# Optimization experiments

Measured on AMD Instinct MI355X. Metric: run time of the kernel, lower is better.

## Reference

```python
import jax, jax.numpy as jnp
import numpy as np

N_USER = 100000
N_ITEM = 50000
EMB = 64
LAYERS = 3
N_INTER = 2000000
BATCH = 4096


def setup_inputs() -> dict:
    key = jax.random.key(0)
    ks = jax.random.split(key, 12)
    N = N_USER + N_ITEM
    # bipartite interactions u -> i, symmetrized
    u = jax.random.randint(ks[0], (N_INTER,), 0, N_USER, dtype=jnp.int32)
    i = jax.random.randint(ks[1], (N_INTER,), 0, N_ITEM, dtype=jnp.int32) + N_USER
    edge_src = jnp.concatenate([u, i])
    edge_dst = jnp.concatenate([i, u])
    # symmetric normalization D^-1/2 A D^-1/2 (as in getSparseGraph)
    deg = jnp.bincount(edge_dst, length=N).astype(jnp.float32)
    d_inv_sqrt = jnp.where(deg > 0, jax.lax.rsqrt(jnp.maximum(deg, 1.0)), 0.0)
    edge_w = d_inv_sqrt[edge_src] * d_inv_sqrt[edge_dst]
    s = 1.0 / np.sqrt(EMB)  # xavier-ish scale
    inp = {
        "user_emb": jax.random.normal(ks[2], (N_USER, EMB), jnp.float32) * s,
        "item_emb": jax.random.normal(ks[3], (N_ITEM, EMB), jnp.float32) * s,
        "W_gc": jax.random.normal(ks[4], (LAYERS, EMB, EMB), jnp.float32) * s,
        "b_gc": jax.random.normal(ks[5], (LAYERS, 1, EMB), jnp.float32) * s,
        "W_bi": jax.random.normal(ks[6], (LAYERS, EMB, EMB), jnp.float32) * s,
        "b_bi": jax.random.normal(ks[7], (LAYERS, 1, EMB), jnp.float32) * s,
        "edge_w": edge_w,
        "edge_src": edge_src,
        "edge_dst": edge_dst,
        "users": jax.random.randint(ks[8], (BATCH,), 0, N_USER, dtype=jnp.int64),
        "pos_items": jax.random.randint(ks[9], (BATCH,), 0, N_ITEM, dtype=jnp.int64),
        "neg_items": jax.random.randint(ks[10], (BATCH,), 0, N_ITEM, dtype=jnp.int64),
    }
    return inp


def reference(user_emb, item_emb, W_gc, b_gc, W_bi, b_bi, edge_w,
              edge_src, edge_dst, users, pos_items, neg_items):
    n_user = user_emb.shape[0]
    N = n_user + item_emb.shape[0]
    ego = jnp.concatenate([user_emb, item_emb], axis=0)  # [N, d]
    all_embeddings = [ego]
    for k in range(W_gc.shape[0]):
        # SpMM: side = A_hat @ ego  (gather + weighted scatter-add)
        side = jax.ops.segment_sum(ego[edge_src] * edge_w[:, None], edge_dst,
                                   num_segments=N)
        sum_e = side @ W_gc[k] + b_gc[k]
        bi_e = (ego * side) @ W_bi[k] + b_bi[k]
        ego = jax.nn.leaky_relu(sum_e + bi_e, negative_slope=0.2)
        # dropout omitted (eval mode / identity for deterministic baseline)
        nrm = jnp.linalg.norm(ego, axis=1, keepdims=True)
        all_embeddings.append(ego / jnp.maximum(nrm, 1e-12))
    all_e = jnp.concatenate(all_embeddings, axis=1)  # [N, (L+1)*d]
    u_g = all_e[:n_user][users]
    i_g = all_e[n_user:]
    return (u_g, i_g[pos_items], i_g[neg_items])
```

## Files before the change

kernel.cpp:

```cpp
#include <hip/hip_runtime.h>

#define EMB 64
#define B2SHIFT 8
#define B2ROWS 256
#define MAXB 1024

typedef short v8s __attribute__((ext_vector_type(8)));
typedef float v4f __attribute__((ext_vector_type(4)));

__device__ __forceinline__ float b2f(unsigned short u) {
    return __uint_as_float(((unsigned int)u) << 16);
}
__device__ __forceinline__ unsigned short f2b(float f) {
    unsigned int u = __float_as_uint(f);
    u += 0x7FFF + ((u >> 16) & 1);
    return (unsigned short)(u >> 16);
}

__global__ void k_init_ego(const float* __restrict__ user_emb,
                           const float* __restrict__ item_emb,
                           const float* __restrict__ dsq,
                           unsigned short* __restrict__ egob,
                           unsigned short* __restrict__ egow,
                           unsigned short* __restrict__ all_eb,
                           int n_user, int N) {
    int idx = blockIdx.x * blockDim.x + threadIdx.x;
    int total = N * EMB;
    if (idx >= total) return;
    int n = idx >> 6;
    int c = idx & 63;
    float v = (n < n_user) ? user_emb[idx] : item_emb[(size_t)(n - n_user) * EMB + c];
    unsigned short b = f2b(v);
    egob[idx] = b;
    egow[idx] = f2b(dsq[n] * v);
    __builtin_nontemporal_store(b, &all_eb[(size_t)n * 256 + c]);
}

__global__ __launch_bounds__(256) void k_bhist(const int* __restrict__ dst,
                                               int* __restrict__ bins,
                                               int M, int nb2) {
    __shared__ int h[MAXB];
    for (int i = threadIdx.x; i < nb2; i += 256) h[i] = 0;
    __syncthreads();
    for (int e = blockIdx.x * 256 + threadIdx.x; e < M; e += gridDim.x * 256)
        atomicAdd(&h[dst[e] >> B2SHIFT], 1);
    __syncthreads();
    for (int i = threadIdx.x; i < nb2; i += 256)
        if (h[i]) atomicAdd(&bins[i], h[i]);
}

__global__ __launch_bounds__(1024) void k_bscan(const int* __restrict__ bins,
                                                int* __restrict__ boff,
                                                int* __restrict__ bcur,
                                                int* __restrict__ row_ptr,
                                                int P, int N) {
    __shared__ int buf[1024];
    int tid = threadIdx.x;
    int v = (tid < P) ? bins[tid] : 0;
    buf[tid] = v;
    __syncthreads();
    for (int d = 1; d < 1024; d <<= 1) {
        int add = (tid >= d) ? buf[tid - d] : 0;
        __syncthreads();
        buf[tid] += add;
        __syncthreads();
    }
    if (tid < P) {
        int excl = buf[tid] - v;
        boff[tid] = excl;
        bcur[tid] = excl;
    }
    if (tid == P - 1) {
        boff[P] = buf[tid];
        row_ptr[N] = buf[tid];
    }
}

__global__ __launch_bounds__(256) void k_bin(const int* __restrict__ src,
                                             const int* __restrict__ dst,
                                             int* __restrict__ bcur,
                                             int* __restrict__ binned,
                                             int M, int nb2) {
    __shared__ int hist[MAXB];
    __shared__ int runcur[MAXB];
    int chunk = (M + gridDim.x - 1) / gridDim.x;
    int lo = blockIdx.x * chunk;
    int hi = min(lo + chunk, M);
    for (int i = threadIdx.x; i < nb2; i += 256) hist[i] = 0;
    __syncthreads();
    for (int e = lo + threadIdx.x; e < hi; e += 256)
        atomicAdd(&hist[dst[e] >> B2SHIFT], 1);
    __syncthreads();
    for (int i = threadIdx.x; i < nb2; i += 256) {
        int c = hist[i];
        runcur[i] = c ? atomicAdd(&bcur[i], c) : 0;
    }
    __syncthreads();
    for (int e = lo + threadIdx.x; e < hi; e += 256) {
        int d = dst[e];
        int pos = atomicAdd(&runcur[d >> B2SHIFT], 1);
        binned[pos] = (src[e] << B2SHIFT) | (d & (B2ROWS - 1));
    }
}

__global__ __launch_bounds__(256) void k_csrb(const int* __restrict__ boff,
                                              const int* __restrict__ binned,
                                              int* __restrict__ row_ptr,
                                              float* __restrict__ dsq,
                                              int* __restrict__ csr, int N) {
    __shared__ int hist[B2ROWS];
    __shared__ int scan[B2ROWS];
    int b = blockIdx.x;
    int beg = boff[b], end = boff[b + 1];
    int tid = threadIdx.x;
    hist[tid] = 0;
    __syncthreads();
    for (int e = beg + tid; e < end; e += 256)
        atomicAdd(&hist[binned[e] & (B2ROWS - 1)], 1);
    __syncthreads();
    int c = hist[tid];
    scan[tid] = c;
    __syncthreads();
    for (int d = 1; d < B2ROWS; d <<= 1) {
        int add = (tid >= d) ? scan[tid - d] : 0;
        __syncthreads();
        scan[tid] += add;
        __syncthreads();
    }
    int excl = beg + scan[tid] - c;
    int node = (b << B2SHIFT) + tid;
    if (node < N) {
        row_ptr[node] = excl;
        dsq[node] = (c > 0) ? rsqrtf((float)c) : 0.0f;
    }
    __syncthreads();
    hist[tid] = excl;
    __syncthreads();
    for (int e = beg + tid; e < end; e += 256) {
        int v = binned[e];
        int pos = atomicAdd(&hist[v & (B2ROWS - 1)], 1);
        csr[pos] = v >> B2SHIFT;
    }
}

__global__ __launch_bounds__(256) void k_side(const int* __restrict__ row_ptr,
                                              const int* __restrict__ csr,
                                              const float* __restrict__ dsq,
                                              const unsigned short* __restrict__ egow,
                                              const unsigned short* __restrict__ egob,
                                              unsigned short* __restrict__ X, int N) {
    int wave = threadIdx.x >> 6;
    int lane = threadIdx.x & 63;
    int n = blockIdx.x * 4 + wave;
    if (n >= N) return;
    int beg = __builtin_amdgcn_readfirstlane(row_ptr[n]);
    int end = __builtin_amdgcn_readfirstlane(row_ptr[n + 1]);
    float a0 = 0.f, a1 = 0.f, a2 = 0.f, a3 = 0.f;
    int e = beg;
    while (e < end) {
        int take = end - e;
        if (take > 64) take = 64;
        int vidx = csr[min(e + lane, end - 1)];
        int j = 0;
        for (; j + 16 <= take; j += 16) {
            int s[16];
#pragma unroll
            for (int u = 0; u < 16; u++)
                s[u] = __builtin_amdgcn_readlane(vidx, j + u);
            float v[16];
#pragma unroll
            for (int u = 0; u < 16; u++)
                v[u] = b2f(egow[(size_t)s[u] * EMB + lane]);
#pragma unroll
            for (int u = 0; u < 16; u += 4) {
                a0 += v[u + 0];
                a1 += v[u + 1];
                a2 += v[u + 2];
                a3 += v[u + 3];
            }
        }
        for (; j + 8 <= take; j += 8) {
            int s0 = __builtin_amdgcn_readlane(vidx, j + 0);
            int s1 = __builtin_amdgcn_readlane(vidx, j + 1);
            int s2 = __builtin_amdgcn_readlane(vidx, j + 2);
            int s3 = __builtin_amdgcn_readlane(vidx, j + 3);
            int s4 = __builtin_amdgcn_readlane(vidx, j + 4);
            int s5 = __builtin_amdgcn_readlane(vidx, j + 5);
            int s6 = __builtin_amdgcn_readlane(vidx, j + 6);
            int s7 = __builtin_amdgcn_readlane(vidx, j + 7);
            float v0 = b2f(egow[(size_t)s0 * EMB + lane]);
            float v1 = b2f(egow[(size_t)s1 * EMB + lane]);
            float v2 = b2f(egow[(size_t)s2 * EMB + lane]);
            float v3 = b2f(egow[(size_t)s3 * EMB + lane]);
            float v4 = b2f(egow[(size_t)s4 * EMB + lane]);
            float v5 = b2f(egow[(size_t)s5 * EMB + lane]);
            float v6 = b2f(egow[(size_t)s6 * EMB + lane]);
            float v7 = b2f(egow[(size_t)s7 * EMB + lane]);
            a0 += v0 + v4;
            a1 += v1 + v5;
            a2 += v2 + v6;
            a3 += v3 + v7;
        }
        for (; j < take; j++) {
            int s = __builtin_amdgcn_readlane(vidx, j);
            a0 += b2f(egow[(size_t)s * EMB + lane]);
        }
        e += take;
    }
    float s = dsq[n] * ((a0 + a1) + (a2 + a3));
    float eg = b2f(egob[(size_t)n * EMB + lane]);
    X[(size_t)n * 128 + lane] = f2b(s);
    X[(size_t)n * 128 + 64 + lane] = f2b(s * eg);
}

__global__ __launch_bounds__(256, 2) void k_mt(
        const unsigned short* __restrict__ X,
        unsigned short* __restrict__ egob, unsigned short* __restrict__ egow,
        const float* __restrict__ dsq,
        const float* __restrict__ Wgc, const float* __restrict__ bgc,
        const float* __restrict__ Wbi, const float* __restrict__ bbi,
        unsigned short* __restrict__ all_eb, int N, int layer_col) {
    __shared__ unsigned short sWT[64 * 136];
    __shared__ float sB[64];
    int tid = threadIdx.x;
    for (int i = tid; i < 64 * 64; i += 256) {
        int k = i >> 6, n = i & 63;
        sWT[n * 136 + k]      = f2b(Wgc[i]);
        sWT[n * 136 + 64 + k] = f2b(Wbi[i]);
    }
    if (tid < 64) sB[tid] = bgc[tid] + bbi[tid];
    __syncthreads();

    int wave = tid >> 6, lane = tid & 63;
    int q = lane >> 4, col = lane & 15;

    v8s Bf[4][4];
#pragma unroll
    for (int nt = 0; nt < 4; nt++)
#pragma unroll
        for (int kt = 0; kt < 4; kt++)
            Bf[nt][kt] = *(const v8s*)&sWT[(nt * 16 + col) * 136 + kt * 32 + q * 8];

    int nrt = (N + 15) >> 4;
    int rt0 = (blockIdx.x * 4 + wave) * 4;
    int rt1 = min(rt0 + 4, nrt);
    for (int t = rt0; t < rt1; t++) {
        int r0 = t << 4;
        int rowA = min(r0 + col, N - 1);
        v8s Af[4];
#pragma unroll
        for (int kt = 0; kt < 4; kt++)
            Af[kt] = *(const v8s*)&X[(size_t)rowA * 128 + kt * 32 + q * 8];
        v4f acc[4];
#pragma unroll
        for (int nt = 0; nt < 4; nt++) {
            float b = sB[nt * 16 + col];
            acc[nt] = (v4f){b, b, b, b};
        }
#pragma unroll
        for (int kt = 0; kt < 4; kt++)
#pragma unroll
            for (int nt = 0; nt < 4; nt++)
                acc[nt] = __builtin_amdgcn_mfma_f32_16x16x32_bf16(
                    Af[kt], Bf[nt][kt], acc[nt], 0, 0, 0);
#pragma unroll
        for (int reg = 0; reg < 4; reg++) {
            int row = r0 + q * 4 + reg;
            float v[4];
            float ssq = 0.f;
#pragma unroll
            for (int nt = 0; nt < 4; nt++) {
                float x = acc[nt][reg];
                x = x > 0.f ? x : 0.2f * x;
                v[nt] = x;
                ssq += x * x;
            }
            ssq += __shfl_xor(ssq, 1, 64);
            ssq += __shfl_xor(ssq, 2, 64);
            ssq += __shfl_xor(ssq, 4, 64);
            ssq += __shfl_xor(ssq, 8, 64);
            float inv = 1.0f / fmaxf(sqrtf(ssq), 1e-12f);
            if (row < N) {
                float dn = dsq[row];
#pragma unroll
                for (int nt = 0; nt < 4; nt++) {
                    int c = nt * 16 + col;
                    egob[(size_t)row * EMB + c] = f2b(v[nt]);
                    egow[(size_t)row * EMB + c] = f2b(v[nt] * dn);
                    __builtin_nontemporal_store(
                        f2b(v[nt] * inv),
                        &all_eb[(size_t)row * 256 + layer_col + c]);
                }
            }
        }
    }
}

__global__ void k_gather(const unsigned short* __restrict__ all_eb,
                         const int* __restrict__ users,
                         const int* __restrict__ pos,
                         const int* __restrict__ neg,
                         float* __restrict__ out, int n_user, int batch) {
    int idx = blockIdx.x * blockDim.x + threadIdx.x;
    int total = batch * 256;
    if (idx >= 3 * total) return;
    int which = idx / total;
    int r = idx - which * total;
    int b = r >> 8;
    int c = r & 255;
    int node;
    if (which == 0) node = users[b];
    else if (which == 1) node = n_user + pos[b];
    else node = n_user + neg[b];
    out[idx] = b2f(all_eb[(size_t)node * 256 + c]);
}

static inline size_t align256(size_t x) { return (x + 255) & ~(size_t)255; }

extern "C" void kernel_launch(void* const* d_in, const int* in_sizes, int n_in,
                              void* d_out, int out_size, void* d_ws, size_t ws_size,
                              hipStream_t stream) {
    const float* user_emb = (const float*)d_in[0];
    const float* item_emb = (const float*)d_in[1];
    const float* W_gc = (const float*)d_in[2];
    const float* b_gc = (const float*)d_in[3];
    const float* W_bi = (const float*)d_in[4];
    const float* b_bi = (const float*)d_in[5];
    const int* edge_src = (const int*)d_in[7];
    const int* edge_dst = (const int*)d_in[8];
    const int* users = (const int*)d_in[9];
    const int* pos = (const int*)d_in[10];
    const int* neg = (const int*)d_in[11];

    int n_user = in_sizes[0] / EMB;
    int n_item = in_sizes[1] / EMB;
    int N = n_user + n_item;
    int M = in_sizes[6];
    int layers = in_sizes[2] / (EMB * EMB);
    int batch = in_sizes[9];
    float* out = (float*)d_out;

    int nb2 = (N + B2ROWS - 1) >> B2SHIFT;
    int nrt = (N + 15) >> 4;

    char* p = (char*)d_ws;
    unsigned short* egob = (unsigned short*)p;   p += align256((size_t)N * EMB * 2);
    unsigned short* egow = (unsigned short*)p;   p += align256((size_t)N * EMB * 2);
    unsigned short* X = (unsigned short*)p;      p += align256((size_t)N * 128 * 2);
    unsigned short* all_eb = (unsigned short*)p; p += align256((size_t)N * 256 * 2);
    float* dsq = (float*)p;            p += align256((size_t)N * 4);
    int* row_ptr = (int*)p;            p += align256((size_t)(N + 1) * 4);
    int* bins = (int*)p;               p += align256((size_t)nb2 * 4);
    int* boff = (int*)p;               p += align256((size_t)(nb2 + 1) * 4);
    int* bcur = (int*)p;               p += align256((size_t)nb2 * 4);
    int* binned = (int*)p;             p += align256((size_t)M * 4);
    int* csr = (int*)p;                p += align256((size_t)M * 4);

    hipMemsetAsync(bins, 0, (size_t)nb2 * 4, stream);

    k_bhist<<<512, 256, 0, stream>>>(edge_dst, bins, M, nb2);
    k_bscan<<<1, 1024, 0, stream>>>(bins, boff, bcur, row_ptr, nb2, N);
    k_bin<<<512, 256, 0, stream>>>(edge_src, edge_dst, bcur, binned, M, nb2);
    k_csrb<<<nb2, 256, 0, stream>>>(boff, binned, row_ptr, dsq, csr, N);

    k_init_ego<<<(N * EMB + 255) / 256, 256, 0, stream>>>(
        user_emb, item_emb, dsq, egob, egow, all_eb, n_user, N);

    for (int k = 0; k < layers; k++) {
        k_side<<<(N + 3) / 4, 256, 0, stream>>>(row_ptr, csr, dsq, egow, egob, X, N);
        k_mt<<<(nrt + 15) / 16, 256, 0, stream>>>(
            X, egob, egow, dsq,
            W_gc + (size_t)k * EMB * EMB, b_gc + (size_t)k * EMB,
            W_bi + (size_t)k * EMB * EMB, b_bi + (size_t)k * EMB,
            all_eb, N, (k + 1) * EMB);
    }

    k_gather<<<(3 * batch * 256 + 255) / 256, 256, 0, stream>>>(
        all_eb, users, pos, neg, out, n_user, batch);
}
```

Measured before the change: 605.7 us.

## Gather four neighbor rows per wave with 8-byte loads in SpMM

The SpMM gather kernel now splits each wave into four 16-lane groups. Each group loads a different neighbor row as uint2 (four bf16 values per lane) instead of each lane loading one 2-byte element of a single row. Partial sums are combined with cross-group shuffles, and 16 lanes write packed outputs. The aim is fewer, wider memory instructions and more gathers in flight, at the cost of shuffles, masking for partial groups, and a final reduction.

```diff
diff --git a/kernel.cpp b/kernel.cpp
--- a/kernel.cpp
+++ b/kernel.cpp
@@ -10,6 +10,12 @@
 
 __device__ __forceinline__ float b2f(unsigned short u) {
     return __uint_as_float(((unsigned int)u) << 16);
+}
+__device__ __forceinline__ float b2f_lo(unsigned int u) {
+    return __uint_as_float(u << 16);
+}
+__device__ __forceinline__ float b2f_hi(unsigned int u) {
+    return __uint_as_float(u & 0xFFFF0000u);
 }
 __device__ __forceinline__ unsigned short f2b(float f) {
     unsigned int u = __float_as_uint(f);
@@ -155,62 +161,64 @@
     if (n >= N) return;
     int beg = __builtin_amdgcn_readfirstlane(row_ptr[n]);
     int end = __builtin_amdgcn_readfirstlane(row_ptr[n + 1]);
+    int g = lane >> 4;
+    int l15 = lane & 15;
+    const uint2* __restrict__ egow2 = (const uint2*)egow;
     float a0 = 0.f, a1 = 0.f, a2 = 0.f, a3 = 0.f;
     int e = beg;
     while (e < end) {
         int take = end - e;
         if (take > 64) take = 64;
         int vidx = csr[min(e + lane, end - 1)];
-        int j = 0;
-        for (; j + 16 <= take; j += 16) {
-            int s[16];
-#pragma unroll
-            for (int u = 0; u < 16; u++)
-                s[u] = __builtin_amdgcn_readlane(vidx, j + u);
-            float v[16];
-#pragma unroll
-            for (int u = 0; u < 16; u++)
-                v[u] = b2f(egow[(size_t)s[u] * EMB + lane]);
-#pragma unroll
-            for (int u = 0; u < 16; u += 4) {
-                a0 += v[u + 0];
-                a1 += v[u + 1];
-                a2 += v[u + 2];
-                a3 += v[u + 3];
+        int ng = (take + 3) >> 2;
+        uint2 u[16];
+#pragma unroll
+        for (int t = 0; t < 16; t++) {
+            if (t < ng) {
+                int jj = t * 4 + g;
+                jj = jj < take ? jj : take - 1;
+                int s = __shfl(vidx, jj);
+                u[t] = egow2[(unsigned)s * 16u + (unsigned)l15];
             }
         }
-        for (; j + 8 <= take; j += 8) {
-            int s0 = __builtin_amdgcn_readlane(vidx, j + 0);
-            int s1 = __builtin_amdgcn_readlane(vidx, j + 1);
-            int s2 = __builtin_amdgcn_readlane(vidx, j + 2);
-            int s3 = __builtin_amdgcn_readlane(vidx, j + 3);
-            int s4 = __builtin_amdgcn_readlane(vidx, j + 4);
-            int s5 = __builtin_amdgcn_readlane(vidx, j + 5);
-            int s6 = __builtin_amdgcn_readlane(vidx, j + 6);
-            int s7 = __builtin_amdgcn_readlane(vidx, j + 7);
-            float v0 = b2f(egow[(size_t)s0 * EMB + lane]);
-            float v1 = b2f(egow[(size_t)s1 * EMB + lane]);
-            float v2 = b2f(egow[(size_t)s2 * EMB + lane]);
-            float v3 = b2f(egow[(size_t)s3 * EMB + lane]);
-            float v4 = b2f(egow[(size_t)s4 * EMB + lane]);
-            float v5 = b2f(egow[(size_t)s5 * EMB + lane]);
-            float v6 = b2f(egow[(size_t)s6 * EMB + lane]);
-            float v7 = b2f(egow[(size_t)s7 * EMB + lane]);
-            a0 += v0 + v4;
-            a1 += v1 + v5;
-            a2 += v2 + v6;
-            a3 += v3 + v7;
-        }
-        for (; j < take; j++) {
-            int s = __builtin_amdgcn_readlane(vidx, j);
-            a0 += b2f(egow[(size_t)s * EMB + lane]);
+#pragma unroll
+        for (int t = 0; t < 16; t++) {
+            if (t < ng) {
+                unsigned ux = u[t].x, uy = u[t].y;
+                bool valid = (t * 4 + g) < take;
+                ux = valid ? ux : 0u;
+                uy = valid ? uy : 0u;
+                a0 += b2f_lo(ux);
+                a1 += b2f_hi(ux);
+                a2 += b2f_lo(uy);
+                a3 += b2f_hi(uy);
+            }
         }
         e += take;
     }
-    float s = dsq[n] * ((a0 + a1) + (a2 + a3));
-    float eg = b2f(egob[(size_t)n * EMB + lane]);
-    X[(size_t)n * 128 + lane] = f2b(s);
-    X[(size_t)n * 128 + 64 + lane] = f2b(s * eg);
+    a0 += __shfl_xor(a0, 16, 64);
+    a0 += __shfl_xor(a0, 32, 64);
+    a1 += __shfl_xor(a1, 16, 64);
+    a1 += __shfl_xor(a1, 32, 64);
+    a2 += __shfl_xor(a2, 16, 64);
+    a2 += __shfl_xor(a2, 32, 64);
+    a3 += __shfl_xor(a3, 16, 64);
+    a3 += __shfl_xor(a3, 32, 64);
+    float d = dsq[n];
+    float s0 = d * a0, s1 = d * a1, s2 = d * a2, s3 = d * a3;
+    if (lane < 16) {
+        const uint2 eg = *(const uint2*)&egob[(size_t)n * EMB + l15 * 4];
+        uint2 p0;
+        p0.x = (unsigned)f2b(s0) | ((unsigned)f2b(s1) << 16);
+        p0.y = (unsigned)f2b(s2) | ((unsigned)f2b(s3) << 16);
+        *(uint2*)&X[(size_t)n * 128 + l15 * 4] = p0;
+        float e0 = b2f_lo(eg.x), e1 = b2f_hi(eg.x);
+        float e2 = b2f_lo(eg.y), e3 = b2f_hi(eg.y);
+        uint2 p1;
+        p1.x = (unsigned)f2b(s0 * e0) | ((unsigned)f2b(s1 * e1) << 16);
+        p1.y = (unsigned)f2b(s2 * e2) | ((unsigned)f2b(s3 * e3) << 16);
+        *(uint2*)&X[(size_t)n * 128 + 64 + l15 * 4] = p1;
+    }
 }
 
 __global__ __launch_bounds__(256, 2) void k_mt(
```

Result: slower. 635.8 us (+5.0%).
